# Kernel tuning notes

Measured on AMD Instinct MI355X. Metric: run time of the kernel, lower is better.

The kernel has to match this reference:

```python
import jax, jax.numpy as jnp
import numpy as np

COMMITMENT_COST = 0.25

def setup_inputs() -> dict:
    key = jax.random.key(0)
    k1, k2 = jax.random.split(key)
    inputs = jax.random.normal(k1, (16, 256, 64, 64), dtype=jnp.float32)   # [B, C=D, H, W]
    embedding = jax.random.normal(k2, (2048, 256), dtype=jnp.float32)      # [K, D] codebook
    return {"inputs": inputs, "embedding": embedding}

def reference(inputs, embedding):
    K, D = embedding.shape
    x = jnp.transpose(inputs, (0, 2, 3, 1))            # [B, H, W, D]
    flat = x.reshape(-1, D)                            # [N, D]
    distances = (jnp.sum(flat * flat, axis=1, keepdims=True)
                 + jnp.sum(embedding * embedding, axis=1)
                 - 2.0 * flat @ embedding.T)
    idx = jnp.argmin(distances, axis=1)                # [N]
    encodings = jax.nn.one_hot(idx, K, dtype=flat.dtype)  # [N, K]
    quantized = embedding[idx].reshape(x.shape)        # gather == one_hot @ embedding
    # commitment loss (eval mode: only e_latent term, scaled)
    e_latent_loss = jnp.mean((jax.lax.stop_gradient(quantized) - x) ** 2)
    loss = COMMITMENT_COST * e_latent_loss
    # straight-through estimator
    quantized_st = x + jax.lax.stop_gradient(quantized - x)
    avg_probs = jnp.mean(encodings, axis=0)
    perplexity = jnp.exp(-jnp.sum(avg_probs * jnp.log(avg_probs + 1e-10)))
    return (loss,
            jnp.transpose(quantized_st, (0, 3, 1, 2)),  # back to [B, C, H, W]
            perplexity,
            encodings)
```

## Files before the change

kernel.cpp:

```cpp
#include <hip/hip_runtime.h>

#define KCODES  2048
#define DDIM    256

#define OUT_LOSS 0
#define OUT_Q    1
#define OUT_PERP 16777217
#define OUT_ENC  16777218

#define WS_IDX  0
#define WS_E2   1048576
#define WS_CNT  1056768
#define WS_SUM  1064960
#define WS_EHI  2097152

typedef _Float16 f16x8 __attribute__((ext_vector_type(8)));
typedef _Float16 f16x4 __attribute__((ext_vector_type(4)));
typedef float    f32x4 __attribute__((ext_vector_type(4)));
typedef float    f32x2 __attribute__((ext_vector_type(2)));

__device__ __forceinline__ void gld16(const void* g, void* l) {
    __builtin_amdgcn_global_load_lds((const __attribute__((address_space(1))) void*)g,
                                     (__attribute__((address_space(3))) void*)l, 16, 0, 0);
}

#define MERGE2(m1,i1,m2,i2,n1,j1,n2,j2)                                   \
    {                                                                     \
        const bool w_ = ((n1) < (m1)) || ((n1) == (m1) && (j1) < (i1));   \
        const float w1_ = w_ ? (n1) : (m1); const int wi_ = w_ ? (j1) : (i1); \
        const float l1_ = w_ ? (m1) : (n1); const int li_ = w_ ? (i1) : (j1); \
        const float c2_ = w_ ? (n2) : (m2); const int ci_ = w_ ? (j2) : (i2); \
        const bool s_ = ((c2_) < (l1_)) || ((c2_) == (l1_) && (ci_) < (li_)); \
        (m1) = w1_; (i1) = wi_;                                           \
        (m2) = s_ ? c2_ : l1_; (i2) = s_ ? ci_ : li_;                     \
    }

__launch_bounds__(256)
__global__ void k_e2split(const float* __restrict__ emb, _Float16* __restrict__ Ehi,
                          float* __restrict__ e2, int* __restrict__ counts,
                          float* __restrict__ sumsq) {
    const int wave = threadIdx.x >> 6;
    const int lane = threadIdx.x & 63;
    const int k = blockIdx.x * 4 + wave;
    const float4 v = *(const float4*)(emb + k * DDIM + lane * 4);
    f16x4 h;
    h[0] = (_Float16)v.x; h[1] = (_Float16)v.y; h[2] = (_Float16)v.z; h[3] = (_Float16)v.w;
    *(f16x4*)(Ehi + k * DDIM + lane * 4) = h;
    float s = v.x * v.x + v.y * v.y + v.z * v.z + v.w * v.w;
#pragma unroll
    for (int off = 32; off >= 1; off >>= 1) s += __shfl_down(s, off);
    if (lane == 0) e2[k] = s;
    if (blockIdx.x < 8) counts[blockIdx.x * 256 + threadIdx.x] = 0;
    if (blockIdx.x == 8 && threadIdx.x == 0) sumsq[0] = 0.0f;
}

__launch_bounds__(256, 2)
__global__ void k_main(const float* __restrict__ inp, const float* __restrict__ emb,
                       const _Float16* __restrict__ Ehi, const float* __restrict__ e2g,
                       int* __restrict__ idx_g, int* __restrict__ counts,
                       float* __restrict__ sumsq) {
    __shared__ __align__(16) char pool[81920];
    _Float16* A  = (_Float16*)pool;
    _Float16* Bh = (_Float16*)(pool + 65536);

    const int rb  = blockIdx.x;
    const int b   = rb >> 5;
    const int hw0 = (rb & 31) << 7;
    const int n0  = rb << 7;
    const int tid = threadIdx.x;
    const int w = tid >> 6, lane = tid & 63;
    const int lq = lane >> 4, lm = lane & 15;
    const int wr = (w >> 1) * 64, wc = (w & 1) * 64;
    const int r8 = lane >> 3, c8 = lane & 7;
    const int gch = c8 ^ r8;

    const float* base = inp + (size_t)b * 1048576 + hw0;
#pragma unroll 4
    for (int rr = 0; rr < 16; ++rr) {
        const int row = ((rr & 1) << 6) + lane;
        const int cg  = ((rr >> 1) << 2) + w;
        const float* p = base + (size_t)(cg << 3) * 4096 + row;
        float v[8];
#pragma unroll
        for (int j = 0; j < 8; ++j) v[j] = p[(size_t)j * 4096];
        f16x8 h;
#pragma unroll
        for (int j = 0; j < 8; ++j) h[j] = (_Float16)v[j];
        const int q  = cg >> 3;
        const int ch = cg & 7;
        *(f16x8*)&A[row * 256 + q * 64 + ((ch ^ (row & 7)) << 3)] = h;
    }
    __syncthreads();

    const int sw0 = ((lq    ) ^ (lm & 7)) << 3;
    const int sw1 = ((lq ^ 4) ^ (lm & 7)) << 3;

    float V1[4][4], V2[4][4]; int I1[4][4], I2[4][4];
#pragma unroll
    for (int i = 0; i < 4; ++i)
#pragma unroll
        for (int rr = 0; rr < 4; ++rr) {
            V1[i][rr] = 3.402823466e38f; V2[i][rr] = 3.402823466e38f;
            I1[i][rr] = 0x7fffffff;      I2[i][rr] = 0x7fffffff;
        }

#pragma unroll 1
    for (int ct = 0; ct < 16; ++ct) {
        const int c0 = ct * 128;
        float e2v[4];
#pragma unroll
        for (int j = 0; j < 4; ++j) e2v[j] = e2g[c0 + wc + j * 16 + lm];

        f32x4 acc[4][4];
#pragma unroll
        for (int i = 0; i < 4; ++i)
#pragma unroll
            for (int j = 0; j < 4; ++j) acc[i][j] = (f32x4)(0.0f);

#pragma unroll 1
        for (int kt = 0; kt < 4; ++kt) {
            const int d0 = kt * 64;
            __syncthreads();
#pragma unroll
            for (int i = 0; i < 4; ++i) {
                const int Row = i * 32 + w * 8 + r8;
                gld16(Ehi + (size_t)(c0 + Row) * DDIM + d0 + gch * 8, &Bh[(i * 32 + w * 8) * 64]);
            }
            __syncthreads();
#pragma unroll
            for (int s = 0; s < 2; ++s) {
                const int wch = s * 4 + lq;
                const int sw = s ? sw1 : sw0;
                f16x8 af[4], bf[4];
#pragma unroll
                for (int t = 0; t < 4; ++t) {
                    const int Rb = wc + t * 16 + lm;
                    af[t] = *(const f16x8*)&A[(wr + t * 16 + lm) * 256 + d0 + sw];
                    bf[t] = *(const f16x8*)&Bh[Rb * 64 + ((wch ^ (Rb & 7)) << 3)];
                }
#pragma unroll
                for (int i = 0; i < 4; ++i)
#pragma unroll
                    for (int j = 0; j < 4; ++j)
                        acc[i][j] = __builtin_amdgcn_mfma_f32_16x16x32_f16(af[i], bf[j], acc[i][j], 0, 0, 0);
            }
        }

#pragma unroll
        for (int i = 0; i < 4; ++i)
#pragma unroll
            for (int j = 0; j < 4; ++j) {
                const int idx = c0 + wc + j * 16 + lm;
#pragma unroll
                for (int rr = 0; rr < 4; ++rr) {
                    const float dist = fmaf(-2.0f, acc[i][j][rr], e2v[j]);
                    const bool b1 = dist < V1[i][rr];
                    const bool b2 = dist < V2[i][rr];
                    V2[i][rr] = b1 ? V1[i][rr] : (b2 ? dist : V2[i][rr]);
                    I2[i][rr] = b1 ? I1[i][rr] : (b2 ? idx  : I2[i][rr]);
                    V1[i][rr] = b1 ? dist : V1[i][rr];
                    I1[i][rr] = b1 ? idx  : I1[i][rr];
                }
            }
    }

    __syncthreads();
    float4* red  = (float4*)pool;
    float*  lsum = (float*)(pool + 4096);
    float*  xf   = (float*)(pool + 8192);
#pragma unroll
    for (int i = 0; i < 4; ++i)
#pragma unroll
        for (int rr = 0; rr < 4; ++rr) {
            float m1 = V1[i][rr]; int i1 = I1[i][rr];
            float m2 = V2[i][rr]; int i2 = I2[i][rr];
#pragma unroll
            for (int off = 1; off < 16; off <<= 1) {
                const float n1 = __shfl_xor(m1, off); const int j1 = __shfl_xor(i1, off);
                const float n2 = __shfl_xor(m2, off); const int j2 = __shfl_xor(i2, off);
                MERGE2(m1, i1, m2, i2, n1, j1, n2, j2);
            }
            if (lm == 0) {
                const int row = wr + i * 16 + lq * 4 + rr;
                red[row * 2 + (w & 1)] = make_float4(m1, __int_as_float(i1),
                                                     m2, __int_as_float(i2));
            }
        }
    if (tid == 0) *lsum = 0.f;

    const int g16 = tid >> 4;
    float Sp[8][4], X2r[8];
#pragma unroll
    for (int rr = 0; rr < 8; ++rr) {
        X2r[rr] = 0.f;
#pragma unroll
        for (int c = 0; c < 4; ++c) Sp[rr][c] = 0.f;
    }

#pragma unroll 1
    for (int h = 0; h < 2; ++h) {
        __syncthreads();
#pragma unroll 8
        for (int k2 = 0; k2 < 32; ++k2) {
            const int dloc = w * 32 + k2;
            const float* sp = base + (size_t)(h * 128 + dloc) * 4096;
            xf[dloc * 129 + lane]      = sp[lane];
            xf[dloc * 129 + 64 + lane] = sp[64 + lane];
        }
        __syncthreads();
#pragma unroll
        for (int rr = 0; rr < 8; ++rr) {
            const int r = g16 * 8 + rr;
            const float4 Ac = red[r * 2];
            const float4 Bc = red[r * 2 + 1];
            const int cid[4] = {__float_as_int(Ac.y), __float_as_int(Ac.w),
                                __float_as_int(Bc.y), __float_as_int(Bc.w)};
            float x8[8];
#pragma unroll
            for (int j = 0; j < 8; ++j) x8[j] = xf[(lm * 8 + j) * 129 + r];
#pragma unroll
            for (int j = 0; j < 8; ++j) X2r[rr] = fmaf(x8[j], x8[j], X2r[rr]);
#pragma unroll
            for (int c = 0; c < 4; ++c) {
                const float* ep = emb + (size_t)cid[c] * DDIM + h * 128 + lm * 8;
                const float4 e0 = *(const float4*)ep;
                const float4 e1 = *(const float4*)(ep + 4);
                float s = Sp[rr][c];
                s = fmaf(x8[0], e0.x, s); s = fmaf(x8[1], e0.y, s);
                s = fmaf(x8[2], e0.z, s); s = fmaf(x8[3], e0.w, s);
                s = fmaf(x8[4], e1.x, s); s = fmaf(x8[5], e1.y, s);
                s = fmaf(x8[6], e1.z, s); s = fmaf(x8[7], e1.w, s);
                Sp[rr][c] = s;
            }
        }
    }

    float lracc = 0.f;
#pragma unroll
    for (int rr = 0; rr < 8; ++rr) {
        const int r = g16 * 8 + rr;
        float s0 = Sp[rr][0], s1 = Sp[rr][1], s2 = Sp[rr][2], s3 = Sp[rr][3];
        float x2v = X2r[rr];
#pragma unroll
        for (int off = 1; off < 16; off <<= 1) {
            s0 += __shfl_xor(s0, off); s1 += __shfl_xor(s1, off);
            s2 += __shfl_xor(s2, off); s3 += __shfl_xor(s3, off);
            x2v += __shfl_xor(x2v, off);
        }
        const float4 Ac = red[r * 2];
        const float4 Bc = red[r * 2 + 1];
        const int cid[4] = {__float_as_int(Ac.y), __float_as_int(Ac.w),
                            __float_as_int(Bc.y), __float_as_int(Bc.w)};
        const float S4[4] = {s0, s1, s2, s3};
        float bv = 3.402823466e38f; int bi = 0; float sb = 0.f, eb = 0.f;
#pragma unroll
        for (int k = 0; k < 4; ++k) {
            const float ev = e2g[cid[k]];
            const float dv = fmaf(-2.0f, S4[k], ev);
            if (dv < bv || (dv == bv && cid[k] < bi)) { bv = dv; bi = cid[k]; sb = S4[k]; eb = ev; }
        }
        if (lm == rr) {
            idx_g[n0 + r] = bi;
            atomicAdd(&counts[bi], 1);
            lracc = x2v - 2.0f * sb + eb;
        }
    }
#pragma unroll
    for (int off = 32; off >= 1; off >>= 1) lracc += __shfl_down(lracc, off);
    if (lane == 0) atomicAdd(lsum, lracc);
    __syncthreads();
    if (tid == 0) atomicAdd(sumsq, *lsum);
}

__launch_bounds__(256)
__global__ void k_out(const float* __restrict__ emb, const int* __restrict__ idx_g,
                      float* __restrict__ outQ, float* __restrict__ enc) {
    __shared__ __align__(16) float Qs[32][260];
    __shared__ int idxs[32];
    const int blk = blockIdx.x;
    const int b   = blk >> 7;
    const int hw0 = (blk & 127) << 5;
    const int tid = threadIdx.x;
    const int w = tid >> 6, lane = tid & 63;
    const int g = tid >> 4, lm = tid & 15;
    const int n0 = (b << 12) + hw0;

    if (tid < 32) idxs[tid] = idx_g[n0 + tid];
    __syncthreads();

#pragma unroll
    for (int rr = 0; rr < 2; ++rr) {
        const int r = g * 2 + rr;
        const float* ep = emb + (size_t)idxs[r] * DDIM + lm * 16;
#pragma unroll
        for (int j = 0; j < 4; ++j)
            *(float4*)&Qs[r][lm * 16 + j * 4] = *(const float4*)(ep + j * 4);
    }
    __syncthreads();

    float* op = outQ + (size_t)b * 1048576 + hw0;
    const int dh = lane >> 5, hl = lane & 31;
#pragma unroll 8
    for (int dd = 0; dd < 32; ++dd) {
        const int d = w * 64 + dd * 2 + dh;
        __builtin_nontemporal_store(Qs[hl][d], op + (size_t)d * 4096 + hl);
    }

    f32x2* erow = (f32x2*)enc + (size_t)n0 * 1024;
#pragma unroll 1
    for (int rr = 0; rr < 32; ++rr) {
        const int id = idxs[rr];
        f32x2* rp = erow + (size_t)rr * 1024;
#pragma unroll
        for (int k = 0; k < 4; ++k) {
            const int c2 = k * 256 + tid;
            const int ccc = c2 * 2;
            f32x2 v;
            v[0] = (ccc == id) ? 1.0f : 0.0f;
            v[1] = (ccc + 1 == id) ? 1.0f : 0.0f;
            __builtin_nontemporal_store(v, rp + c2);
        }
    }
}

__launch_bounds__(256)
__global__ void k_finalize(const int* __restrict__ counts, const float* __restrict__ sumsq,
                           float* __restrict__ out) {
    __shared__ float red[256];
    const int t = threadIdx.x;
    float s = 0.0f;
    for (int k = t; k < KCODES; k += 256) {
        const float p = (float)counts[k] * (1.0f / 65536.0f);
        s += p * logf(p + 1e-10f);
    }
    red[t] = s;
    __syncthreads();
    for (int off = 128; off >= 1; off >>= 1) {
        if (t < off) red[t] += red[t + off];
        __syncthreads();
    }
    if (t == 0) {
        out[OUT_PERP] = expf(-red[0]);
        out[OUT_LOSS] = 0.25f * sumsq[0] * (1.0f / 16777216.0f);
    }
}

extern "C" void kernel_launch(void* const* d_in, const int* in_sizes, int n_in,
                              void* d_out, int out_size, void* d_ws, size_t ws_size,
                              hipStream_t stream) {
    const float* inp = (const float*)d_in[0];
    const float* emb = (const float*)d_in[1];
    float* out = (float*)d_out;
    char* wsb  = (char*)d_ws;

    int*      idxg   = (int*)(wsb + WS_IDX);
    float*    e2     = (float*)(wsb + WS_E2);
    int*      counts = (int*)(wsb + WS_CNT);
    float*    sumsq  = (float*)(wsb + WS_SUM);
    _Float16* Ehi    = (_Float16*)(wsb + WS_EHI);

    k_e2split <<<512,  256, 0, stream>>>(emb, Ehi, e2, counts, sumsq);
    k_main    <<<512,  256, 0, stream>>>(inp, emb, Ehi, e2, idxg, counts, sumsq);
    k_out     <<<2048, 256, 0, stream>>>(emb, idxg, out + OUT_Q, out + OUT_ENC);
    k_finalize<<<1,    256, 0, stream>>>(counts, sumsq, out);
}
```

Before: 858.0 us.

## Fuse output writing into main kernel, drop separate output kernel

The one-hot encoding writes and the quantized gather/transpose writes move into the end of k_main. The argmin indices are kept in shared memory instead of a global index buffer. This removes one kernel launch and the global round trip for the indices, and lets the large output stores overlap with other blocks' compute. In exchange, only 512 blocks now issue the output stores, with lower occupancy (launch bounds 256,2 and a large LDS footprint), which could reduce store parallelism compared with the 2048-block kernel.

```diff
diff --git a/kernel.cpp b/kernel.cpp
--- a/kernel.cpp
+++ b/kernel.cpp
@@ -8,7 +8,6 @@
 #define OUT_PERP 16777217
 #define OUT_ENC  16777218
 
-#define WS_IDX  0
 #define WS_E2   1048576
 #define WS_CNT  1056768
 #define WS_SUM  1064960
@@ -57,8 +56,8 @@
 __launch_bounds__(256, 2)
 __global__ void k_main(const float* __restrict__ inp, const float* __restrict__ emb,
                        const _Float16* __restrict__ Ehi, const float* __restrict__ e2g,
-                       int* __restrict__ idx_g, int* __restrict__ counts,
-                       float* __restrict__ sumsq) {
+                       int* __restrict__ counts, float* __restrict__ sumsq,
+                       float* __restrict__ outQ, float* __restrict__ encQ) {
     __shared__ __align__(16) char pool[81920];
     _Float16* A  = (_Float16*)pool;
     _Float16* Bh = (_Float16*)(pool + 65536);
@@ -166,7 +165,8 @@
 
     __syncthreads();
     float4* red  = (float4*)pool;
-    float*  lsum = (float*)(pool + 4096);
+    int*    idxs = (int*)(pool + 4096);
+    float*  lsum = (float*)(pool + 4608);
     float*  xf   = (float*)(pool + 8192);
 #pragma unroll
     for (int i = 0; i < 4; ++i)
@@ -260,7 +260,7 @@
             if (dv < bv || (dv == bv && cid[k] < bi)) { bv = dv; bi = cid[k]; sb = S4[k]; eb = ev; }
         }
         if (lm == rr) {
-            idx_g[n0 + r] = bi;
+            idxs[r] = bi;
             atomicAdd(&counts[bi], 1);
             lracc = x2v - 2.0f * sb + eb;
         }
@@ -270,45 +270,10 @@
     if (lane == 0) atomicAdd(lsum, lracc);
     __syncthreads();
     if (tid == 0) atomicAdd(sumsq, *lsum);
-}
-
-__launch_bounds__(256)
-__global__ void k_out(const float* __restrict__ emb, const int* __restrict__ idx_g,
-                      float* __restrict__ outQ, float* __restrict__ enc) {
-    __shared__ __align__(16) float Qs[32][260];
-    __shared__ int idxs[32];
-    const int blk = blockIdx.x;
-    const int b   = blk >> 7;
-    const int hw0 = (blk & 127) << 5;
-    const int tid = threadIdx.x;
-    const int w = tid >> 6, lane = tid & 63;
-    const int g = tid >> 4, lm = tid & 15;
-    const int n0 = (b << 12) + hw0;
-
-    if (tid < 32) idxs[tid] = idx_g[n0 + tid];
-    __syncthreads();
-
-#pragma unroll
-    for (int rr = 0; rr < 2; ++rr) {
-        const int r = g * 2 + rr;
-        const float* ep = emb + (size_t)idxs[r] * DDIM + lm * 16;
-#pragma unroll
-        for (int j = 0; j < 4; ++j)
-            *(float4*)&Qs[r][lm * 16 + j * 4] = *(const float4*)(ep + j * 4);
-    }
-    __syncthreads();
-
-    float* op = outQ + (size_t)b * 1048576 + hw0;
-    const int dh = lane >> 5, hl = lane & 31;
-#pragma unroll 8
-    for (int dd = 0; dd < 32; ++dd) {
-        const int d = w * 64 + dd * 2 + dh;
-        __builtin_nontemporal_store(Qs[hl][d], op + (size_t)d * 4096 + hl);
-    }
-
-    f32x2* erow = (f32x2*)enc + (size_t)n0 * 1024;
-#pragma unroll 1
-    for (int rr = 0; rr < 32; ++rr) {
+
+    f32x2* erow = (f32x2*)encQ + (size_t)n0 * 1024;
+#pragma unroll 1
+    for (int rr = 0; rr < 128; ++rr) {
         const int id = idxs[rr];
         f32x2* rp = erow + (size_t)rr * 1024;
 #pragma unroll
@@ -319,6 +284,29 @@
             v[0] = (ccc == id) ? 1.0f : 0.0f;
             v[1] = (ccc + 1 == id) ? 1.0f : 0.0f;
             __builtin_nontemporal_store(v, rp + c2);
+        }
+    }
+
+    float* Qs = (float*)(pool + 8192);
+    const int gq = tid >> 4, lmq = tid & 15;
+#pragma unroll 1
+    for (int c = 0; c < 4; ++c) {
+        __syncthreads();
+#pragma unroll
+        for (int rr2 = 0; rr2 < 2; ++rr2) {
+            const int rl = gq * 2 + rr2;
+            const float* ep = emb + (size_t)idxs[c * 32 + rl] * DDIM + lmq * 16;
+#pragma unroll
+            for (int j = 0; j < 4; ++j)
+                *(float4*)&Qs[rl * 260 + lmq * 16 + j * 4] = *(const float4*)(ep + j * 4);
+        }
+        __syncthreads();
+        float* op = outQ + (size_t)b * 1048576 + hw0 + c * 32;
+        const int dh = lane >> 5, hl = lane & 31;
+#pragma unroll 8
+        for (int dd = 0; dd < 32; ++dd) {
+            const int d = w * 64 + dd * 2 + dh;
+            __builtin_nontemporal_store(Qs[hl * 260 + d], op + (size_t)d * 4096 + hl);
         }
     }
 }
@@ -353,14 +341,13 @@
     float* out = (float*)d_out;
     char* wsb  = (char*)d_ws;
 
-    int*      idxg   = (int*)(wsb + WS_IDX);
     float*    e2     = (float*)(wsb + WS_E2);
     int*      counts = (int*)(wsb + WS_CNT);
     float*    sumsq  = (float*)(wsb + WS_SUM);
     _Float16* Ehi    = (_Float16*)(wsb + WS_EHI);
 
-    k_e2split <<<512,  256, 0, stream>>>(emb, Ehi, e2, counts, sumsq);
-    k_main    <<<512,  256, 0, stream>>>(inp, emb, Ehi, e2, idxg, counts, sumsq);
-    k_out     <<<2048, 256, 0, stream>>>(emb, idxg, out + OUT_Q, out + OUT_ENC);
-    k_finalize<<<1,    256, 0, stream>>>(counts, sumsq, out);
-}
+    k_e2split <<<512, 256, 0, stream>>>(emb, Ehi, e2, counts, sumsq);
+    k_main    <<<512, 256, 0, stream>>>(inp, emb, Ehi, e2, counts, sumsq,
+                                        out + OUT_Q, out + OUT_ENC);
+    k_finalize<<<1,   256, 0, stream>>>(counts, sumsq, out);
+}
```

After: 854.0 us. No clear change (-0.5%).
